# Optimization experiments

Measured on AMD Instinct MI355X. Metric: run time of the kernel, lower is better.

## Reference

```python
import jax, jax.numpy as jnp
import numpy as np

EPS = 1e-5
B, H, W = 256, 64, 64
HASH_NUM, SPLIT_NUM, IN_CH = 48, 16, 3


def conv(x, w, b):
    y = jax.lax.conv_general_dilated(x, w, (1, 1), 'VALID',
                                     dimension_numbers=('NCHW', 'OIHW', 'NCHW'))
    return y + b[None, :, None, None]


def bn2d(x, g, b):
    m = x.mean((0, 2, 3), keepdims=True)
    v = x.var((0, 2, 3), keepdims=True)
    return (x - m) * jax.lax.rsqrt(v + EPS) * g[None, :, None, None] + b[None, :, None, None]


def bn1d(x, g, b):
    m = x.mean(0)
    v = x.var(0)
    return (x - m) * jax.lax.rsqrt(v + EPS) * g + b


def maxpool2(x):
    return jax.lax.reduce_window(x, -jnp.inf, jax.lax.max,
                                 (1, 1, 2, 2), (1, 1, 2, 2), 'VALID')


def setup_inputs() -> dict:
    key = jax.random.key(0)
    ks = jax.random.split(key, 16)
    s = 0.1
    inp = {
        'x': jax.random.normal(ks[0], (B, IN_CH, H, W), jnp.float32),
        'conv1_w': jax.random.normal(ks[1], (20, IN_CH, 3, 3), jnp.float32) * s,
        'conv1_b': jnp.zeros((20,), jnp.float32),
        'bn1_g': jnp.ones((20,), jnp.float32),
        'bn1_b': jnp.zeros((20,), jnp.float32),
        'conv2_w': jax.random.normal(ks[2], (40, 20, 2, 2), jnp.float32) * s,
        'conv2_b': jnp.zeros((40,), jnp.float32),
        'bn2_g': jnp.ones((40,), jnp.float32),
        'bn2_b': jnp.zeros((40,), jnp.float32),
        'conv3_w': jax.random.normal(ks[3], (60, 40, 2, 2), jnp.float32) * s,
        'conv3_b': jnp.zeros((60,), jnp.float32),
        'bn3_g': jnp.ones((60,), jnp.float32),
        'bn3_b': jnp.zeros((60,), jnp.float32),
        # LocallyConnected2d: weight [1, 80, 60, 6, 6, 4], bias [1, 80, 6, 6]
        'lc_w': jax.random.normal(ks[4], (1, 80, 60, 6, 6, 4), jnp.float32) * s,
        'lc_b': jax.random.normal(ks[5], (1, 80, 6, 6), jnp.float32) * s,
        'bn4_g': jnp.ones((80,), jnp.float32),
        'bn4_b': jnp.zeros((80,), jnp.float32),
        # Linear(5820 -> 768): torch stores weight as [out, in]
        'fc_w': jax.random.normal(ks[6], (HASH_NUM * SPLIT_NUM, 5820), jnp.float32) * 0.01,
        'fc_b': jnp.zeros((HASH_NUM * SPLIT_NUM,), jnp.float32),
        'bn5_g': jnp.ones((HASH_NUM * SPLIT_NUM,), jnp.float32),
        'bn5_b': jnp.zeros((HASH_NUM * SPLIT_NUM,), jnp.float32),
        # per-hash fuse linears Linear(split_num, 1), stacked -> [48, 16], [48]
        'fuse_w': jax.random.normal(ks[7], (HASH_NUM, SPLIT_NUM), jnp.float32) * s,
        'fuse_b': jnp.zeros((HASH_NUM,), jnp.float32),
    }
    return inp


def reference(x, conv1_w, conv1_b, bn1_g, bn1_b,
              conv2_w, conv2_b, bn2_g, bn2_b,
              conv3_w, conv3_b, bn3_g, bn3_b,
              lc_w, lc_b, bn4_g, bn4_b,
              fc_w, fc_b, bn5_g, bn5_b,
              fuse_w, fuse_b):
    h = maxpool2(jax.nn.relu(bn2d(conv(x, conv1_w, conv1_b), bn1_g, bn1_b)))   # [B,20,31,31]
    h = maxpool2(jax.nn.relu(bn2d(conv(h, conv2_w, conv2_b), bn2_g, bn2_b)))   # [B,40,15,15]
    h = maxpool2(jax.nn.relu(bn2d(conv(h, conv3_w, conv3_b), bn3_g, bn3_b)))   # [B,60,7,7]
    x1 = h.reshape(h.shape[0], -1)                                             # [B,2940]
    # LocallyConnected2d k=2, s=1: patches [B,60,6,6,4], flatten order (kh,kw)
    p = jnp.stack([h[:, :, 0:6, 0:6], h[:, :, 0:6, 1:7],
                   h[:, :, 1:7, 0:6], h[:, :, 1:7, 1:7]], axis=-1)
    lc = jnp.einsum('bcijk,ocijk->boij', p, lc_w[0]) + lc_b                    # [B,80,6,6]
    lc = jax.nn.relu(bn2d(lc, bn4_g, bn4_b))
    x2 = lc.reshape(lc.shape[0], -1)                                           # [B,2880]
    feat = jnp.concatenate([x1, x2], axis=1)                                   # [B,5820]
    y = feat @ fc_w.T + fc_b                                                   # [B,768]
    y = jax.nn.relu(bn1d(y, bn5_g, bn5_b))
    yr = y.reshape(y.shape[0], HASH_NUM, SPLIT_NUM)                            # [B,48,16]
    out = jnp.einsum('bhs,hs->bh', yr, fuse_w) + fuse_b                        # [B,48]
    return out
```

## Files before the change

### kernel.cpp

```cpp
#include <hip/hip_runtime.h>

#define EPSF 1e-5f

#define P1S 0
#define P1Q 81920
#define P2S 163840
#define P2Q 204800
#define P3S 245760
#define P3Q 261120
#define P4S 276480
#define P4Q 279360
#define SC1 282240
#define SH1 282260
#define SC2 282280
#define SH2 282320
#define SC3 282360
#define SH3 282420
#define SC4 282480
#define SH4 282560
#define SC5 282640
#define SH5 283408

#define OFF_A 524288
#define OFF_B 20205568
#define OFF_C 25125888
#define OFF_D 25878528
#define OFF_Y 26615808

#define KP 6144

__device__ __forceinline__ void blockReduce2(float& v1, float& v2) {
  __syncthreads();
  #pragma unroll
  for (int off = 32; off > 0; off >>= 1) {
    v1 += __shfl_down(v1, off);
    v2 += __shfl_down(v2, off);
  }
  __shared__ float s1[4], s2[4];
  const int wid = threadIdx.x >> 6, lane = threadIdx.x & 63;
  if (lane == 0) { s1[wid] = v1; s2[wid] = v2; }
  __syncthreads();
  if (threadIdx.x == 0) { v1 = s1[0]+s1[1]+s1[2]+s1[3]; v2 = s2[0]+s2[1]+s2[2]+s2[3]; }
}

__device__ __forceinline__ void waveReduce2(float& a, float& b) {
  #pragma unroll
  for (int off = 32; off > 0; off >>= 1) {
    a += __shfl_down(a, off);
    b += __shfl_down(b, off);
  }
}

__device__ __forceinline__ unsigned short f2bf(float f) {
  unsigned int u = __float_as_uint(f);
  return (unsigned short)((u + 0x7FFFu + ((u >> 16) & 1u)) >> 16);
}

__global__ __launch_bounds__(256) void conv1_stats_kernel(
    const float* __restrict__ x, const float* __restrict__ w, const float* __restrict__ cb,
    float* __restrict__ ps, float* __restrict__ pq) {
  const int sp = blockIdx.x * 256 + threadIdx.x;
  const int c0 = blockIdx.y * 5, b = blockIdx.z;
  __shared__ float wsh[5][27];
  if (threadIdx.x < 135) wsh[threadIdx.x / 27][threadIdx.x % 27] = w[c0 * 27 + threadIdx.x];
  __syncthreads();
  float s[5] = {}, q[5] = {};
  if (sp < 961) {
    const int py = sp / 31, px = sp - py * 31;
    const float* xb = x + (size_t)b * 3 * 4096 + (2 * py) * 64 + 2 * px;
    float acc[5][4] = {};
    #pragma unroll
    for (int ic = 0; ic < 3; ic++) {
      float v[4][4];
      #pragma unroll
      for (int r = 0; r < 4; r++)
        #pragma unroll
        for (int cc = 0; cc < 4; cc++)
          v[r][cc] = xb[ic * 4096 + r * 64 + cc];
      #pragma unroll
      for (int ol = 0; ol < 5; ol++)
        #pragma unroll
        for (int dy = 0; dy < 2; dy++)
          #pragma unroll
          for (int dx = 0; dx < 2; dx++) {
            float a = acc[ol][dy * 2 + dx];
            #pragma unroll
            for (int ky = 0; ky < 3; ky++)
              #pragma unroll
              for (int kx = 0; kx < 3; kx++)
                a = fmaf(v[dy + ky][dx + kx], wsh[ol][(ic * 3 + ky) * 3 + kx], a);
            acc[ol][dy * 2 + dx] = a;
          }
    }
    #pragma unroll
    for (int ol = 0; ol < 5; ol++) {
      const float base = cb[c0 + ol];
      #pragma unroll
      for (int k = 0; k < 4; k++) {
        const float vv = acc[ol][k] + base;
        s[ol] += vv; q[ol] += vv * vv;
      }
    }
  }
  #pragma unroll
  for (int ol = 0; ol < 5; ol++) waveReduce2(s[ol], q[ol]);
  const int lane = threadIdx.x & 63, wid = threadIdx.x >> 6;
  if (lane == 0) {
    const int slot = b * 16 + blockIdx.x * 4 + wid;
    #pragma unroll
    for (int ol = 0; ol < 5; ol++) {
      ps[(c0 + ol) * 4096 + slot] = s[ol];
      pq[(c0 + ol) * 4096 + slot] = q[ol];
    }
  }
}

__global__ __launch_bounds__(256) void convpool1_kernel(
    const float* __restrict__ x, const float* __restrict__ w, const float* __restrict__ cb,
    const float* __restrict__ scale, const float* __restrict__ shift,
    float* __restrict__ out) {
  const int sp = blockIdx.x * 256 + threadIdx.x;
  const int c0 = blockIdx.y * 5, b = blockIdx.z;
  __shared__ float wsh[5][27];
  if (threadIdx.x < 135) wsh[threadIdx.x / 27][threadIdx.x % 27] = w[c0 * 27 + threadIdx.x];
  __syncthreads();
  if (sp >= 961) return;
  const int py = sp / 31, px = sp - py * 31;
  const float* xb = x + (size_t)b * 3 * 4096 + (2 * py) * 64 + 2 * px;
  float acc[5][4] = {};
  #pragma unroll
  for (int ic = 0; ic < 3; ic++) {
    float v[4][4];
    #pragma unroll
    for (int r = 0; r < 4; r++)
      #pragma unroll
      for (int cc = 0; cc < 4; cc++)
        v[r][cc] = xb[ic * 4096 + r * 64 + cc];
    #pragma unroll
    for (int ol = 0; ol < 5; ol++)
      #pragma unroll
      for (int dy = 0; dy < 2; dy++)
        #pragma unroll
        for (int dx = 0; dx < 2; dx++) {
          float a = acc[ol][dy * 2 + dx];
          #pragma unroll
          for (int ky = 0; ky < 3; ky++)
            #pragma unroll
            for (int kx = 0; kx < 3; kx++)
              a = fmaf(v[dy + ky][dx + kx], wsh[ol][(ic * 3 + ky) * 3 + kx], a);
          acc[ol][dy * 2 + dx] = a;
        }
  }
  #pragma unroll
  for (int ol = 0; ol < 5; ol++) {
    const float sc = scale[c0 + ol];
    const float sh = fmaf(cb[c0 + ol], sc, shift[c0 + ol]);
    float m = -1e30f;
    #pragma unroll
    for (int k = 0; k < 4; k++)
      m = fmaxf(m, fmaxf(fmaf(acc[ol][k], sc, sh), 0.f));
    out[(size_t)(b * 20 + c0 + ol) * 961 + sp] = m;
  }
}

__global__ __launch_bounds__(256) void conv2_stats_kernel(
    const float* __restrict__ in, const float* __restrict__ w, const float* __restrict__ cb,
    float* __restrict__ ps, float* __restrict__ pq) {
  const int sp = threadIdx.x;
  const int c0 = blockIdx.y * 8, b = blockIdx.z;
  __shared__ float4 wsh4[8][20];
  for (int e = threadIdx.x; e < 160; e += 256)
    wsh4[e / 20][e % 20] = ((const float4*)w)[c0 * 20 + e];
  __syncthreads();
  float s[8] = {}, q[8] = {};
  if (sp < 225) {
    const int py = sp / 15, px = sp - py * 15;
    const float* ib = in + (size_t)b * 20 * 961 + (2 * py) * 31 + 2 * px;
    float acc[8][4] = {};
    #pragma unroll 4
    for (int ic = 0; ic < 20; ic++) {
      float v[3][3];
      #pragma unroll
      for (int r = 0; r < 3; r++)
        #pragma unroll
        for (int cc = 0; cc < 3; cc++)
          v[r][cc] = ib[ic * 961 + r * 31 + cc];
      #pragma unroll
      for (int ol = 0; ol < 8; ol++) {
        const float4 wv = wsh4[ol][ic];
        #pragma unroll
        for (int dy = 0; dy < 2; dy++)
          #pragma unroll
          for (int dx = 0; dx < 2; dx++) {
            float a = acc[ol][dy * 2 + dx];
            a = fmaf(v[dy][dx],     wv.x, a);
            a = fmaf(v[dy][dx + 1], wv.y, a);
            a = fmaf(v[dy + 1][dx], wv.z, a);
            a = fmaf(v[dy + 1][dx + 1], wv.w, a);
            acc[ol][dy * 2 + dx] = a;
          }
      }
    }
    #pragma unroll
    for (int ol = 0; ol < 8; ol++) {
      const float base = cb[c0 + ol];
      #pragma unroll
      for (int k = 0; k < 4; k++) {
        const float vv = acc[ol][k] + base;
        s[ol] += vv; q[ol] += vv * vv;
      }
    }
  }
  #pragma unroll
  for (int ol = 0; ol < 8; ol++) waveReduce2(s[ol], q[ol]);
  const int lane = threadIdx.x & 63, wid = threadIdx.x >> 6;
  if (lane == 0) {
    const int slot = b * 4 + wid;
    #pragma unroll
    for (int ol = 0; ol < 8; ol++) {
      ps[(c0 + ol) * 1024 + slot] = s[ol];
      pq[(c0 + ol) * 1024 + slot] = q[ol];
    }
  }
}

__global__ __launch_bounds__(256) void convpool2_kernel(
    const float* __restrict__ in, const float* __restrict__ w, const float* __restrict__ cb,
    const float* __restrict__ scale, const float* __restrict__ shift,
    float* __restrict__ out) {
  const int sp = threadIdx.x;
  const int c0 = blockIdx.y * 8, b = blockIdx.z;
  __shared__ float4 wsh4[8][20];
  for (int e = threadIdx.x; e < 160; e += 256)
    wsh4[e / 20][e % 20] = ((const float4*)w)[c0 * 20 + e];
  __syncthreads();
  if (sp >= 225) return;
  const int py = sp / 15, px = sp - py * 15;
  const float* ib = in + (size_t)b * 20 * 961 + (2 * py) * 31 + 2 * px;
  float acc[8][4] = {};
  #pragma unroll 4
  for (int ic = 0; ic < 20; ic++) {
    float v[3][3];
    #pragma unroll
    for (int r = 0; r < 3; r++)
      #pragma unroll
      for (int cc = 0; cc < 3; cc++)
        v[r][cc] = ib[ic * 961 + r * 31 + cc];
    #pragma unroll
    for (int ol = 0; ol < 8; ol++) {
      const float4 wv = wsh4[ol][ic];
      #pragma unroll
      for (int dy = 0; dy < 2; dy++)
        #pragma unroll
        for (int dx = 0; dx < 2; dx++) {
          float a = acc[ol][dy * 2 + dx];
          a = fmaf(v[dy][dx],     wv.x, a);
          a = fmaf(v[dy][dx + 1], wv.y, a);
          a = fmaf(v[dy + 1][dx], wv.z, a);
          a = fmaf(v[dy + 1][dx + 1], wv.w, a);
          acc[ol][dy * 2 + dx] = a;
        }
    }
  }
  #pragma unroll
  for (int ol = 0; ol < 8; ol++) {
    const float sc = scale[c0 + ol];
    const float sh = fmaf(cb[c0 + ol], sc, shift[c0 + ol]);
    float m = -1e30f;
    #pragma unroll
    for (int k = 0; k < 4; k++)
      m = fmaxf(m, fmaxf(fmaf(acc[ol][k], sc, sh), 0.f));
    out[(size_t)(b * 40 + c0 + ol) * 225 + sp] = m;
  }
}

__global__ __launch_bounds__(256) void conv3_kernel(
    const float* __restrict__ in, const float* __restrict__ w, const float* __restrict__ cb,
    float* __restrict__ out, float* __restrict__ ps, float* __restrict__ pq) {
  const int sp = threadIdx.x;
  const int c0 = blockIdx.y * 6, b = blockIdx.z;
  __shared__ float4 wsh4[6][40];
  if (threadIdx.x < 240)
    wsh4[threadIdx.x / 40][threadIdx.x % 40] = ((const float4*)w)[c0 * 40 + threadIdx.x];
  __syncthreads();
  float acc[6] = {};
  if (sp < 196) {
    const int oy = sp / 14, ox = sp - oy * 14;
    const float* ib = in + (size_t)b * 40 * 225 + oy * 15 + ox;
    #pragma unroll 4
    for (int ic = 0; ic < 40; ic++) {
      const float v0 = ib[ic * 225];
      const float v1 = ib[ic * 225 + 1];
      const float v2 = ib[ic * 225 + 15];
      const float v3 = ib[ic * 225 + 16];
      #pragma unroll
      for (int ol = 0; ol < 6; ol++) {
        const float4 wv = wsh4[ol][ic];
        acc[ol] = fmaf(v0, wv.x, acc[ol]);
        acc[ol] = fmaf(v1, wv.y, acc[ol]);
        acc[ol] = fmaf(v2, wv.z, acc[ol]);
        acc[ol] = fmaf(v3, wv.w, acc[ol]);
      }
    }
    #pragma unroll
    for (int ol = 0; ol < 6; ol++) {
      acc[ol] += cb[c0 + ol];
      out[(size_t)(b * 60 + c0 + ol) * 196 + sp] = acc[ol];
    }
  }
  #pragma unroll
  for (int ol = 0; ol < 6; ol++) {
    float v1 = acc[ol], v2 = acc[ol] * acc[ol];
    blockReduce2(v1, v2);
    if (threadIdx.x == 0) {
      ps[(c0 + ol) * 256 + b] = v1;
      pq[(c0 + ol) * 256 + b] = v2;
    }
  }
}

template<int SLOTS>
__global__ __launch_bounds__(256) void bnfin_kernel(
    const float* __restrict__ ps, const float* __restrict__ pq,
    const float* __restrict__ g, const float* __restrict__ bet,
    float* __restrict__ scale, float* __restrict__ shift, float invN) {
  const int c = blockIdx.x;
  float s = 0.f, q = 0.f;
  for (int i = threadIdx.x; i < SLOTS; i += 256) { s += ps[c * SLOTS + i]; q += pq[c * SLOTS + i]; }
  blockReduce2(s, q);
  if (threadIdx.x == 0) {
    const float m = s * invN;
    const float var = q * invN - m * m;
    const float sc = g[c] * rsqrtf(var + EPSF);
    scale[c] = sc;
    shift[c] = bet[c] - m * sc;
  }
}

template<int C, int Hin, int Win, int Hout, int Wout>
__global__ __launch_bounds__(256) void bnrelupool_kernel(
    const float* __restrict__ in, float* __restrict__ out,
    const float* __restrict__ scale, const float* __restrict__ shift, int total) {
  const int idx = blockIdx.x * 256 + threadIdx.x;
  if (idx >= total) return;
  const int px = idx % Wout;
  int t = idx / Wout;
  const int py = t % Hout; t /= Hout;
  const int c = t % C;
  const int b = t / C;
  const float sc = scale[c], sh = shift[c];
  const float* p = in + ((size_t)(b * C + c) * Hin + 2 * py) * Win + 2 * px;
  const float2 r0 = *(const float2*)p;
  const float2 r1 = *(const float2*)(p + Win);
  float a0 = fmaxf(fmaf(r0.x, sc, sh), 0.f);
  float a1 = fmaxf(fmaf(r0.y, sc, sh), 0.f);
  float a2 = fmaxf(fmaf(r1.x, sc, sh), 0.f);
  float a3 = fmaxf(fmaf(r1.y, sc, sh), 0.f);
  out[idx] = fmaxf(fmaxf(a0, a1), fmaxf(a2, a3));
}

__global__ __launch_bounds__(256) void transpose_h_kernel(
    const float* __restrict__ in, float* __restrict__ out) {
  __shared__ float tile[64][65];
  const int lx = threadIdx.x & 63, ly = threadIdx.x >> 6;
  const int c0 = blockIdx.x * 64;
  const int r0 = blockIdx.y * 64;
  #pragma unroll
  for (int i = 0; i < 16; i++) {
    const int b = r0 + ly + i * 4;
    const int cp = c0 + lx;
    tile[ly + i * 4][lx] = (cp < 2940) ? in[(size_t)b * 2940 + cp] : 0.f;
  }
  __syncthreads();
  #pragma unroll
  for (int i = 0; i < 16; i++) {
    const int cp = c0 + ly + i * 4;
    if (cp < 2940) out[(size_t)cp * 256 + r0 + lx] = tile[lx][ly + i * 4];
  }
}

__global__ __launch_bounds__(256) void lc2_kernel(
    const float* __restrict__ hT, const float* __restrict__ w, const float* __restrict__ lb,
    float* __restrict__ outT, float* __restrict__ ps, float* __restrict__ pq) {
  const int sp = blockIdx.x;
  const int o0 = blockIdx.y * 8;
  const int b = threadIdx.x;
  __shared__ float wsh[8 * 240];
  for (int e = threadIdx.x; e < 1920; e += 256) {
    const int ol = e / 240, ck = e - ol * 240;
    const int c = ck >> 2, k = ck & 3;
    wsh[e] = w[((size_t)((o0 + ol) * 60 + c) * 36 + sp) * 4 + k];
  }
  __syncthreads();
  const int i = sp / 6, j = sp - i * 6;
  const int pos0 = i * 7 + j;
  float acc[8] = {};
  #pragma unroll 4
  for (int c = 0; c < 60; c++) {
    const float h0 = hT[(size_t)(c * 49 + pos0) * 256 + b];
    const float h1 = hT[(size_t)(c * 49 + pos0 + 1) * 256 + b];
    const float h2 = hT[(size_t)(c * 49 + pos0 + 7) * 256 + b];
    const float h3 = hT[(size_t)(c * 49 + pos0 + 8) * 256 + b];
    #pragma unroll
    for (int ol = 0; ol < 8; ol++) {
      const float* wp = &wsh[ol * 240 + c * 4];
      acc[ol] = fmaf(h0, wp[0], acc[ol]);
      acc[ol] = fmaf(h1, wp[1], acc[ol]);
      acc[ol] = fmaf(h2, wp[2], acc[ol]);
      acc[ol] = fmaf(h3, wp[3], acc[ol]);
    }
  }
  #pragma unroll
  for (int ol = 0; ol < 8; ol++) {
    const int o = o0 + ol;
    const float val = acc[ol] + lb[o * 36 + sp];
    outT[(size_t)(o * 36 + sp) * 256 + b] = val;
    float v1 = val, v2 = val * val;
    blockReduce2(v1, v2);
    if (threadIdx.x == 0) { ps[o * 36 + sp] = v1; pq[o * 36 + sp] = v2; }
  }
}

__global__ __launch_bounds__(256) void lcpost2_kernel(
    const float* __restrict__ inT, float* __restrict__ out,
    const float* __restrict__ scale, const float* __restrict__ shift) {
  __shared__ float tile[64][65];
  const int lx = threadIdx.x & 63, ly = threadIdx.x >> 6;
  const int k0 = blockIdx.x * 64;
  const int b0 = blockIdx.y * 64;
  #pragma unroll
  for (int i = 0; i < 16; i++) {
    const int k = k0 + ly + i * 4;
    const int o = k / 36;
    const float v = inT[(size_t)k * 256 + b0 + lx];
    tile[ly + i * 4][lx] = fmaxf(fmaf(v, scale[o], shift[o]), 0.f);
  }
  __syncthreads();
  #pragma unroll
  for (int i = 0; i < 16; i++) {
    const int b = b0 + ly + i * 4;
    out[(size_t)b * 2880 + k0 + lx] = tile[lx][ly + i * 4];
  }
}

__global__ __launch_bounds__(256) void pack_feat_kernel(
    const float* __restrict__ h, const float* __restrict__ x2, unsigned short* __restrict__ fB) {
  const int idx = blockIdx.x * 256 + threadIdx.x;
  const int b = idx / 1536, kq = idx - b * 1536;
  const int k0 = kq * 4;
  ushort4 o;
  float v[4];
  #pragma unroll
  for (int q = 0; q < 4; q++) {
    const int k = k0 + q;
    v[q] = (k < 2940) ? h[(size_t)b * 2940 + k]
         : (k < 5820) ? x2[(size_t)b * 2880 + (k - 2940)] : 0.f;
  }
  o.x = f2bf(v[0]); o.y = f2bf(v[1]); o.z = f2bf(v[2]); o.w = f2bf(v[3]);
  *(ushort4*)&fB[(size_t)b * KP + k0] = o;
}

__global__ __launch_bounds__(256) void pack_w_kernel(
    const float* __restrict__ W, unsigned short* __restrict__ WBp) {
  const int idx = blockIdx.x * 256 + threadIdx.x;
  const int n = idx / 1536, kq = idx - n * 1536;
  const int k0 = kq * 4;
  ushort4 o;
  float v[4];
  #pragma unroll
  for (int q = 0; q < 4; q++) {
    const int k = k0 + q;
    v[q] = (k < 5820) ? W[(size_t)n * 5820 + k] : 0.f;
  }
  o.x = f2bf(v[0]); o.y = f2bf(v[1]); o.z = f2bf(v[2]); o.w = f2bf(v[3]);
  *(ushort4*)&WBp[(size_t)n * KP + k0] = o;
}

typedef __attribute__((ext_vector_type(4))) float f32x4;
typedef __attribute__((ext_vector_type(8))) short bf16x8;

__global__ __launch_bounds__(256) void fc_mfma_kernel(
    const unsigned short* __restrict__ fB, const unsigned short* __restrict__ WBp,
    float* __restrict__ Y) {
  const int wid = threadIdx.x >> 6, l = threadIdx.x & 63;
  const int wy = wid >> 1, wx = wid & 1;
  const int m0 = blockIdx.x * 64 + wy * 32;
  const int n0 = blockIdx.y * 64 + wx * 32;
  const int lrow = l & 15, lk = (l >> 4) * 8;
  const unsigned short* ap = fB + (size_t)(m0 + lrow) * KP + lk;
  const unsigned short* bp = WBp + (size_t)(n0 + lrow) * KP + lk;
  f32x4 acc[2][2] = {};
  const int kbase = blockIdx.z * 1536;
  #pragma unroll 4
  for (int s = 0; s < 48; s++) {
    const int k = kbase + s * 32;
    const bf16x8 a0 = *(const bf16x8*)(ap + k);
    const bf16x8 a1 = *(const bf16x8*)(ap + 16 * KP + k);
    const bf16x8 b0 = *(const bf16x8*)(bp + k);
    const bf16x8 b1 = *(const bf16x8*)(bp + 16 * KP + k);
    acc[0][0] = __builtin_amdgcn_mfma_f32_16x16x32_bf16(a0, b0, acc[0][0], 0, 0, 0);
    acc[0][1] = __builtin_amdgcn_mfma_f32_16x16x32_bf16(a0, b1, acc[0][1], 0, 0, 0);
    acc[1][0] = __builtin_amdgcn_mfma_f32_16x16x32_bf16(a1, b0, acc[1][0], 0, 0, 0);
    acc[1][1] = __builtin_amdgcn_mfma_f32_16x16x32_bf16(a1, b1, acc[1][1], 0, 0, 0);
  }
  const int orow = (l >> 4) * 4, ocol = l & 15;
  #pragma unroll
  for (int fi = 0; fi < 2; fi++)
    #pragma unroll
    for (int fj = 0; fj < 2; fj++)
      #pragma unroll
      for (int r = 0; r < 4; r++)
        atomicAdd(&Y[(size_t)(m0 + fi * 16 + orow + r) * 768 + n0 + fj * 16 + ocol],
                  acc[fi][fj][r]);
}

__global__ __launch_bounds__(256) void bn5_stats_kernel(
    const float* __restrict__ Y, const float* __restrict__ g, const float* __restrict__ bet,
    float* __restrict__ scale, float* __restrict__ shift) {
  const int tx = threadIdx.x & 63, ty = threadIdx.x >> 6;
  const int n = blockIdx.x * 64 + tx;
  float s = 0.f, q = 0.f;
  for (int bi = 0; bi < 64; bi++) {
    const float v = Y[(size_t)(bi * 4 + ty) * 768 + n];
    s += v; q += v * v;
  }
  __shared__ float rs[4][64], rq[4][64];
  rs[ty][tx] = s; rq[ty][tx] = q;
  __syncthreads();
  if (ty == 0) {
    s = rs[0][tx] + rs[1][tx] + rs[2][tx] + rs[3][tx];
    q = rq[0][tx] + rq[1][tx] + rq[2][tx] + rq[3][tx];
    const float m = s * (1.f / 256.f);
    const float var = q * (1.f / 256.f) - m * m;
    const float sc = g[n] * rsqrtf(var + EPSF);
    scale[n] = sc;
    shift[n] = bet[n] - m * sc;
  }
}

__global__ __launch_bounds__(256) void final_kernel(
    const float* __restrict__ Y, const float* __restrict__ scale, const float* __restrict__ shift,
    const float* __restrict__ fw, const float* __restrict__ fb, float* __restrict__ out) {
  const int idx = blockIdx.x * 256 + threadIdx.x;
  const int b = idx / 48, hh = idx - b * 48;
  const float* yb = Y + (size_t)b * 768 + hh * 16;
  const float* sc = scale + hh * 16;
  const float* sh = shift + hh * 16;
  const float* w = fw + hh * 16;
  float acc = fb[hh];
  #pragma unroll
  for (int s = 0; s < 16; s++)
    acc += fmaxf(fmaf(yb[s], sc[s], sh[s]), 0.f) * w[s];
  out[idx] = acc;
}

extern "C" void kernel_launch(void* const* d_in, const int* in_sizes, int n_in,
                              void* d_out, int out_size, void* d_ws, size_t ws_size,
                              hipStream_t stream) {
  const float* x   = (const float*)d_in[0];
  const float* c1w = (const float*)d_in[1];
  const float* c1b = (const float*)d_in[2];
  const float* g1  = (const float*)d_in[3];
  const float* b1  = (const float*)d_in[4];
  const float* c2w = (const float*)d_in[5];
  const float* c2b = (const float*)d_in[6];
  const float* g2  = (const float*)d_in[7];
  const float* b2  = (const float*)d_in[8];
  const float* c3w = (const float*)d_in[9];
  const float* c3b = (const float*)d_in[10];
  const float* g3  = (const float*)d_in[11];
  const float* b3  = (const float*)d_in[12];
  const float* lcw = (const float*)d_in[13];
  const float* lcb = (const float*)d_in[14];
  const float* g4  = (const float*)d_in[15];
  const float* b4  = (const float*)d_in[16];
  const float* fcw = (const float*)d_in[17];
  const float* g5  = (const float*)d_in[19];
  const float* b5  = (const float*)d_in[20];
  const float* fw  = (const float*)d_in[21];
  const float* fb  = (const float*)d_in[22];

  float* ws = (float*)d_ws;
  float* A  = ws + OFF_A;
  float* B_ = ws + OFF_B;
  float* C_ = ws + OFF_C;
  float* D_ = ws + OFF_D;
  float* Y  = ws + OFF_Y;
  unsigned short* featB = (unsigned short*)A;
  unsigned short* WB    = (unsigned short*)(A + 786432);

  hipMemsetAsync(Y, 0, 196608 * sizeof(float), stream);

  conv1_stats_kernel<<<dim3(4, 4, 256), 256, 0, stream>>>(x, c1w, c1b, ws + P1S, ws + P1Q);
  bnfin_kernel<4096><<<20, 256, 0, stream>>>(ws + P1S, ws + P1Q, g1, b1, ws + SC1, ws + SH1, 1.f / 984064.f);
  convpool1_kernel<<<dim3(4, 4, 256), 256, 0, stream>>>(x, c1w, c1b, ws + SC1, ws + SH1, B_);
  conv2_stats_kernel<<<dim3(1, 5, 256), 256, 0, stream>>>(B_, c2w, c2b, ws + P2S, ws + P2Q);
  bnfin_kernel<1024><<<40, 256, 0, stream>>>(ws + P2S, ws + P2Q, g2, b2, ws + SC2, ws + SH2, 1.f / 230400.f);
  convpool2_kernel<<<dim3(1, 5, 256), 256, 0, stream>>>(B_, c2w, c2b, ws + SC2, ws + SH2, A);
  conv3_kernel<<<dim3(1, 10, 256), 256, 0, stream>>>(A, c3w, c3b, B_, ws + P3S, ws + P3Q);
  bnfin_kernel<256><<<60, 256, 0, stream>>>(ws + P3S, ws + P3Q, g3, b3, ws + SC3, ws + SH3, 1.f / 50176.f);
  bnrelupool_kernel<60, 14, 14, 7, 7><<<2940, 256, 0, stream>>>(B_, C_, ws + SC3, ws + SH3, 752640);
  transpose_h_kernel<<<dim3(46, 4), 256, 0, stream>>>(C_, B_);
  lc2_kernel<<<dim3(36, 10), 256, 0, stream>>>(B_, lcw, lcb, A, ws + P4S, ws + P4Q);
  bnfin_kernel<36><<<80, 256, 0, stream>>>(ws + P4S, ws + P4Q, g4, b4, ws + SC4, ws + SH4, 1.f / 9216.f);
  lcpost2_kernel<<<dim3(45, 4), 256, 0, stream>>>(A, D_, ws + SC4, ws + SH4);
  pack_feat_kernel<<<1536, 256, 0, stream>>>(C_, D_, featB);
  pack_w_kernel<<<4608, 256, 0, stream>>>(fcw, WB);
  fc_mfma_kernel<<<dim3(4, 12, 4), 256, 0, stream>>>(featB, WB, Y);
  bn5_stats_kernel<<<12, 256, 0, stream>>>(Y, g5, b5, ws + SC5, ws + SH5);
  final_kernel<<<48, 256, 0, stream>>>(Y, ws + SC5, ws + SH5, fw, fb, (float*)d_out);
}
```

Baseline: 362.0 us.

## Fuse conv3 with BN-ReLU-pool via recompute and convert FC weights inside GEMM

Result: slower. 388.8 us (+7.4%).

```diff
diff --git a/kernel.cpp b/kernel.cpp
--- a/kernel.cpp
+++ b/kernel.cpp
@@ -274,48 +274,116 @@
   }
 }
 
-__global__ __launch_bounds__(256) void conv3_kernel(
+__global__ __launch_bounds__(256) void conv3_stats_kernel(
     const float* __restrict__ in, const float* __restrict__ w, const float* __restrict__ cb,
-    float* __restrict__ out, float* __restrict__ ps, float* __restrict__ pq) {
-  const int sp = threadIdx.x;
-  const int c0 = blockIdx.y * 6, b = blockIdx.z;
+    float* __restrict__ ps, float* __restrict__ pq) {
+  const int tid = threadIdx.x;
+  const int c0 = blockIdx.y * 6, bq = blockIdx.z;
   __shared__ float4 wsh4[6][40];
-  if (threadIdx.x < 240)
-    wsh4[threadIdx.x / 40][threadIdx.x % 40] = ((const float4*)w)[c0 * 40 + threadIdx.x];
-  __syncthreads();
-  float acc[6] = {};
-  if (sp < 196) {
-    const int oy = sp / 14, ox = sp - oy * 14;
-    const float* ib = in + (size_t)b * 40 * 225 + oy * 15 + ox;
+  if (tid < 240) wsh4[tid / 40][tid % 40] = ((const float4*)w)[c0 * 40 + tid];
+  __syncthreads();
+  float s[6] = {}, q[6] = {};
+  if (tid < 196) {
+    const int bl = tid / 49, sp = tid - bl * 49;
+    const int b = bq * 4 + bl;
+    const int py = sp / 7, px = sp - py * 7;
+    const float* ib = in + (size_t)b * 40 * 225 + (2 * py) * 15 + 2 * px;
+    float acc[6][4] = {};
     #pragma unroll 4
     for (int ic = 0; ic < 40; ic++) {
-      const float v0 = ib[ic * 225];
-      const float v1 = ib[ic * 225 + 1];
-      const float v2 = ib[ic * 225 + 15];
-      const float v3 = ib[ic * 225 + 16];
+      float v[3][3];
+      #pragma unroll
+      for (int r = 0; r < 3; r++)
+        #pragma unroll
+        for (int cc = 0; cc < 3; cc++)
+          v[r][cc] = ib[ic * 225 + r * 15 + cc];
       #pragma unroll
       for (int ol = 0; ol < 6; ol++) {
         const float4 wv = wsh4[ol][ic];
-        acc[ol] = fmaf(v0, wv.x, acc[ol]);
-        acc[ol] = fmaf(v1, wv.y, acc[ol]);
-        acc[ol] = fmaf(v2, wv.z, acc[ol]);
-        acc[ol] = fmaf(v3, wv.w, acc[ol]);
+        #pragma unroll
+        for (int dy = 0; dy < 2; dy++)
+          #pragma unroll
+          for (int dx = 0; dx < 2; dx++) {
+            float a = acc[ol][dy * 2 + dx];
+            a = fmaf(v[dy][dx],     wv.x, a);
+            a = fmaf(v[dy][dx + 1], wv.y, a);
+            a = fmaf(v[dy + 1][dx], wv.z, a);
+            a = fmaf(v[dy + 1][dx + 1], wv.w, a);
+            acc[ol][dy * 2 + dx] = a;
+          }
       }
     }
     #pragma unroll
     for (int ol = 0; ol < 6; ol++) {
-      acc[ol] += cb[c0 + ol];
-      out[(size_t)(b * 60 + c0 + ol) * 196 + sp] = acc[ol];
+      const float base = cb[c0 + ol];
+      #pragma unroll
+      for (int k = 0; k < 4; k++) {
+        const float vv = acc[ol][k] + base;
+        s[ol] += vv; q[ol] += vv * vv;
+      }
+    }
+  }
+  #pragma unroll
+  for (int ol = 0; ol < 6; ol++) waveReduce2(s[ol], q[ol]);
+  const int lane = threadIdx.x & 63, wid = threadIdx.x >> 6;
+  if (lane == 0) {
+    const int slot = bq * 4 + wid;
+    #pragma unroll
+    for (int ol = 0; ol < 6; ol++) {
+      ps[(c0 + ol) * 256 + slot] = s[ol];
+      pq[(c0 + ol) * 256 + slot] = q[ol];
+    }
+  }
+}
+
+__global__ __launch_bounds__(256) void convpool3_kernel(
+    const float* __restrict__ in, const float* __restrict__ w, const float* __restrict__ cb,
+    const float* __restrict__ scale, const float* __restrict__ shift,
+    float* __restrict__ out) {
+  const int tid = threadIdx.x;
+  const int c0 = blockIdx.y * 6, bq = blockIdx.z;
+  __shared__ float4 wsh4[6][40];
+  if (tid < 240) wsh4[tid / 40][tid % 40] = ((const float4*)w)[c0 * 40 + tid];
+  __syncthreads();
+  if (tid >= 196) return;
+  const int bl = tid / 49, sp = tid - bl * 49;
+  const int b = bq * 4 + bl;
+  const int py = sp / 7, px = sp - py * 7;
+  const float* ib = in + (size_t)b * 40 * 225 + (2 * py) * 15 + 2 * px;
+  float acc[6][4] = {};
+  #pragma unroll 4
+  for (int ic = 0; ic < 40; ic++) {
+    float v[3][3];
+    #pragma unroll
+    for (int r = 0; r < 3; r++)
+      #pragma unroll
+      for (int cc = 0; cc < 3; cc++)
+        v[r][cc] = ib[ic * 225 + r * 15 + cc];
+    #pragma unroll
+    for (int ol = 0; ol < 6; ol++) {
+      const float4 wv = wsh4[ol][ic];
+      #pragma unroll
+      for (int dy = 0; dy < 2; dy++)
+        #pragma unroll
+        for (int dx = 0; dx < 2; dx++) {
+          float a = acc[ol][dy * 2 + dx];
+          a = fmaf(v[dy][dx],     wv.x, a);
+          a = fmaf(v[dy][dx + 1], wv.y, a);
+          a = fmaf(v[dy + 1][dx], wv.z, a);
+          a = fmaf(v[dy + 1][dx + 1], wv.w, a);
+          acc[ol][dy * 2 + dx] = a;
+        }
     }
   }
   #pragma unroll
   for (int ol = 0; ol < 6; ol++) {
-    float v1 = acc[ol], v2 = acc[ol] * acc[ol];
-    blockReduce2(v1, v2);
-    if (threadIdx.x == 0) {
-      ps[(c0 + ol) * 256 + b] = v1;
-      pq[(c0 + ol) * 256 + b] = v2;
-    }
+    const float sc = scale[c0 + ol];
+    const float sh = fmaf(cb[c0 + ol], sc, shift[c0 + ol]);
+    float m = -1e30f;
+    #pragma unroll
+    for (int k = 0; k < 4; k++)
+      m = fmaxf(m, fmaxf(fmaf(acc[ol][k], sc, sh), 0.f));
+    out[(size_t)(b * 60 + c0 + ol) * 49 + sp] = m;
   }
 }
 
@@ -337,28 +405,6 @@
   }
 }
 
-template<int C, int Hin, int Win, int Hout, int Wout>
-__global__ __launch_bounds__(256) void bnrelupool_kernel(
-    const float* __restrict__ in, float* __restrict__ out,
-    const float* __restrict__ scale, const float* __restrict__ shift, int total) {
-  const int idx = blockIdx.x * 256 + threadIdx.x;
-  if (idx >= total) return;
-  const int px = idx % Wout;
-  int t = idx / Wout;
-  const int py = t % Hout; t /= Hout;
-  const int c = t % C;
-  const int b = t / C;
-  const float sc = scale[c], sh = shift[c];
-  const float* p = in + ((size_t)(b * C + c) * Hin + 2 * py) * Win + 2 * px;
-  const float2 r0 = *(const float2*)p;
-  const float2 r1 = *(const float2*)(p + Win);
-  float a0 = fmaxf(fmaf(r0.x, sc, sh), 0.f);
-  float a1 = fmaxf(fmaf(r0.y, sc, sh), 0.f);
-  float a2 = fmaxf(fmaf(r1.x, sc, sh), 0.f);
-  float a3 = fmaxf(fmaf(r1.y, sc, sh), 0.f);
-  out[idx] = fmaxf(fmaxf(a0, a1), fmaxf(a2, a3));
-}
-
 __global__ __launch_bounds__(256) void transpose_h_kernel(
     const float* __restrict__ in, float* __restrict__ out) {
   __shared__ float tile[64][65];
@@ -460,27 +506,30 @@
   *(ushort4*)&fB[(size_t)b * KP + k0] = o;
 }
 
-__global__ __launch_bounds__(256) void pack_w_kernel(
-    const float* __restrict__ W, unsigned short* __restrict__ WBp) {
-  const int idx = blockIdx.x * 256 + threadIdx.x;
-  const int n = idx / 1536, kq = idx - n * 1536;
-  const int k0 = kq * 4;
-  ushort4 o;
-  float v[4];
-  #pragma unroll
-  for (int q = 0; q < 4; q++) {
-    const int k = k0 + q;
-    v[q] = (k < 5820) ? W[(size_t)n * 5820 + k] : 0.f;
-  }
-  o.x = f2bf(v[0]); o.y = f2bf(v[1]); o.z = f2bf(v[2]); o.w = f2bf(v[3]);
-  *(ushort4*)&WBp[(size_t)n * KP + k0] = o;
-}
-
 typedef __attribute__((ext_vector_type(4))) float f32x4;
 typedef __attribute__((ext_vector_type(8))) short bf16x8;
 
+__device__ __forceinline__ bf16x8 ld_w_bf16(const float* __restrict__ row, int kidx) {
+  bf16x8 r;
+  if (kidx + 8 <= 5820) {
+    const float4 f0 = *(const float4*)(row + kidx);
+    const float4 f1 = *(const float4*)(row + kidx + 4);
+    r[0] = (short)f2bf(f0.x); r[1] = (short)f2bf(f0.y);
+    r[2] = (short)f2bf(f0.z); r[3] = (short)f2bf(f0.w);
+    r[4] = (short)f2bf(f1.x); r[5] = (short)f2bf(f1.y);
+    r[6] = (short)f2bf(f1.z); r[7] = (short)f2bf(f1.w);
+  } else {
+    #pragma unroll
+    for (int i = 0; i < 8; i++) {
+      const float v = (kidx + i < 5820) ? row[kidx + i] : 0.f;
+      r[i] = (short)f2bf(v);
+    }
+  }
+  return r;
+}
+
 __global__ __launch_bounds__(256) void fc_mfma_kernel(
-    const unsigned short* __restrict__ fB, const unsigned short* __restrict__ WBp,
+    const unsigned short* __restrict__ fB, const float* __restrict__ W,
     float* __restrict__ Y) {
   const int wid = threadIdx.x >> 6, l = threadIdx.x & 63;
   const int wy = wid >> 1, wx = wid & 1;
@@ -488,16 +537,18 @@
   const int n0 = blockIdx.y * 64 + wx * 32;
   const int lrow = l & 15, lk = (l >> 4) * 8;
   const unsigned short* ap = fB + (size_t)(m0 + lrow) * KP + lk;
-  const unsigned short* bp = WBp + (size_t)(n0 + lrow) * KP + lk;
+  const float* w0 = W + (size_t)(n0 + lrow) * 5820;
+  const float* w1 = W + (size_t)(n0 + lrow + 16) * 5820;
   f32x4 acc[2][2] = {};
   const int kbase = blockIdx.z * 1536;
-  #pragma unroll 4
+  #pragma unroll 2
   for (int s = 0; s < 48; s++) {
     const int k = kbase + s * 32;
+    const int kidx = k + lk;
     const bf16x8 a0 = *(const bf16x8*)(ap + k);
     const bf16x8 a1 = *(const bf16x8*)(ap + 16 * KP + k);
-    const bf16x8 b0 = *(const bf16x8*)(bp + k);
-    const bf16x8 b1 = *(const bf16x8*)(bp + 16 * KP + k);
+    const bf16x8 b0 = ld_w_bf16(w0, kidx);
+    const bf16x8 b1 = ld_w_bf16(w1, kidx);
     acc[0][0] = __builtin_amdgcn_mfma_f32_16x16x32_bf16(a0, b0, acc[0][0], 0, 0, 0);
     acc[0][1] = __builtin_amdgcn_mfma_f32_16x16x32_bf16(a0, b1, acc[0][1], 0, 0, 0);
     acc[1][0] = __builtin_amdgcn_mfma_f32_16x16x32_bf16(a1, b0, acc[1][0], 0, 0, 0);
@@ -587,7 +638,6 @@
   float* D_ = ws + OFF_D;
   float* Y  = ws + OFF_Y;
   unsigned short* featB = (unsigned short*)A;
-  unsigned short* WB    = (unsigned short*)(A + 786432);
 
   hipMemsetAsync(Y, 0, 196608 * sizeof(float), stream);
 
@@ -597,16 +647,15 @@
   conv2_stats_kernel<<<dim3(1, 5, 256), 256, 0, stream>>>(B_, c2w, c2b, ws + P2S, ws + P2Q);
   bnfin_kernel<1024><<<40, 256, 0, stream>>>(ws + P2S, ws + P2Q, g2, b2, ws + SC2, ws + SH2, 1.f / 230400.f);
   convpool2_kernel<<<dim3(1, 5, 256), 256, 0, stream>>>(B_, c2w, c2b, ws + SC2, ws + SH2, A);
-  conv3_kernel<<<dim3(1, 10, 256), 256, 0, stream>>>(A, c3w, c3b, B_, ws + P3S, ws + P3Q);
+  conv3_stats_kernel<<<dim3(1, 10, 64), 256, 0, stream>>>(A, c3w, c3b, ws + P3S, ws + P3Q);
   bnfin_kernel<256><<<60, 256, 0, stream>>>(ws + P3S, ws + P3Q, g3, b3, ws + SC3, ws + SH3, 1.f / 50176.f);
-  bnrelupool_kernel<60, 14, 14, 7, 7><<<2940, 256, 0, stream>>>(B_, C_, ws + SC3, ws + SH3, 752640);
+  convpool3_kernel<<<dim3(1, 10, 64), 256, 0, stream>>>(A, c3w, c3b, ws + SC3, ws + SH3, C_);
   transpose_h_kernel<<<dim3(46, 4), 256, 0, stream>>>(C_, B_);
   lc2_kernel<<<dim3(36, 10), 256, 0, stream>>>(B_, lcw, lcb, A, ws + P4S, ws + P4Q);
   bnfin_kernel<36><<<80, 256, 0, stream>>>(ws + P4S, ws + P4Q, g4, b4, ws + SC4, ws + SH4, 1.f / 9216.f);
   lcpost2_kernel<<<dim3(45, 4), 256, 0, stream>>>(A, D_, ws + SC4, ws + SH4);
   pack_feat_kernel<<<1536, 256, 0, stream>>>(C_, D_, featB);
-  pack_w_kernel<<<4608, 256, 0, stream>>>(fcw, WB);
-  fc_mfma_kernel<<<dim3(4, 12, 4), 256, 0, stream>>>(featB, WB, Y);
+  fc_mfma_kernel<<<dim3(4, 12, 4), 256, 0, stream>>>(featB, fcw, Y);
   bn5_stats_kernel<<<12, 256, 0, stream>>>(Y, g5, b5, ws + SC5, ws + SH5);
   final_kernel<<<48, 256, 0, stream>>>(Y, ws + SC5, ws + SH5, fw, fb, (float*)d_out);
 }
```
